# Kernel optimization log

Hardware: AMD Instinct MI355X
Metric: run time of the kernel (lower is better)

## Reference

```python
import jax, jax.numpy as jnp
import numpy as np

NEG_INF = -1e9
B, D, T_MEL, T_TEXT = 16, 192, 2048, 512


def setup_inputs() -> dict:
    key = jax.random.key(0)
    k1, k2, k3, k4, k5 = jax.random.split(key, 5)
    z_p = jax.random.normal(k1, (B, D, T_MEL), dtype=jnp.float32)
    m_p = jax.random.normal(k2, (B, D, T_TEXT), dtype=jnp.float32)
    logs_p = 0.1 * jax.random.normal(k3, (B, D, T_TEXT), dtype=jnp.float32)
    phoneme_lengths = jax.random.randint(k4, (B,), T_TEXT // 2, T_TEXT + 1, dtype=jnp.int32)
    mel_lengths = jax.random.randint(k5, (B,), T_MEL // 2, T_MEL + 1, dtype=jnp.int32)
    return {"z_p": z_p, "m_p": m_p, "logs_p": logs_p,
            "phoneme_lengths": phoneme_lengths, "mel_lengths": mel_lengths}


def neg_cent_matrix(z_p, m_p, logs_p):
    # z_p: [B,D,Ty] (mel frames), m_p/logs_p: [B,D,Tx] (phonemes)
    s = jnp.exp(-2.0 * logs_p)                                             # 1/sigma^2, [B,D,Tx]
    nc1 = jnp.sum(-0.5 * jnp.log(2.0 * jnp.pi) - logs_p, axis=1, keepdims=True)  # [B,1,Tx]
    nc2 = jnp.einsum('bdy,bdx->byx', -0.5 * z_p * z_p, s)                  # [B,Ty,Tx]
    nc3 = jnp.einsum('bdy,bdx->byx', z_p, m_p * s)                         # [B,Ty,Tx]
    nc4 = jnp.sum(-0.5 * m_p * m_p * s, axis=1, keepdims=True)             # [B,1,Tx]
    return nc1 + nc2 + nc3 + nc4                                           # [B,Ty,Tx]


def maximum_path(neg_cent, t_xs, t_ys):
    """Monotonic alignment search (VITS maximum_path), vmapped over batch.

    neg_cent: [B, T_y, T_x] log-likelihood scores; t_xs/t_ys: valid lengths.
    Returns hard alignment path [B, T_y, T_x] in {0,1}.
    """
    _, T_y, T_x = neg_cent.shape
    x_idx = jnp.arange(T_x)

    def single(value, t_x, t_y):
        # forward DP: cum[y,x] = value[y,x] + max(cum[y-1,x], cum[y-1,x-1])
        init = jnp.where(x_idx == 0, value[0], NEG_INF)

        def fwd_step(prev, v_row):
            shifted = jnp.concatenate([jnp.full((1,), NEG_INF, prev.dtype), prev[:-1]])
            cur = v_row + jnp.maximum(prev, shifted)
            return cur, cur

        _, rest = jax.lax.scan(fwd_step, init, value[1:])
        cum = jnp.concatenate([init[None, :], rest], axis=0)               # [T_y,T_x]

        # backtrack from (t_y-1, t_x-1); rows with y >= t_y are inactive (zeros)
        def bwd_step(index, y):
            active = y < t_y
            row = ((x_idx == index) & active).astype(value.dtype)
            prev_row = cum[jnp.maximum(y - 1, 0)]
            move = (index == y) | (prev_row[index] < prev_row[jnp.maximum(index - 1, 0)])
            move = move & (index > 0) & active & (y > 0)
            nxt = jnp.where(active, index - move.astype(index.dtype), index)
            return nxt, row

        _, rows = jax.lax.scan(bwd_step, t_x - 1, jnp.arange(T_y)[::-1])
        return rows[::-1]

    return jax.vmap(single)(neg_cent, t_xs, t_ys)


def reference(z_p, m_p, logs_p, phoneme_lengths, mel_lengths):
    neg_cent = neg_cent_matrix(z_p, m_p, logs_p)                           # [B,Ty,Tx]
    attn = maximum_path(neg_cent, phoneme_lengths, mel_lengths)            # [B,Ty,Tx]
    T_x = m_p.shape[-1]
    ph_mask = (jnp.arange(T_x)[None, :] < phoneme_lengths[:, None]).astype(z_p.dtype)[:, None, :]  # [B,1,Tx]
    w = jnp.sum(attn, axis=1)[:, None, :]                                  # durations, [B,1,Tx]
    logw_ = jnp.log(w + 1e-6) * ph_mask                                    # [B,1,Tx]
    return neg_cent, attn, logw_
```

## Files before the change

### kernel.cpp

```cpp
#include <hip/hip_runtime.h>
#include <cstdint>
#include <cstddef>

#define B_   16
#define D_   192
#define TY   2048
#define TX   512
#define NEG_INF_F (-1e9f)

#define CHUNK 16
#define RING  4
#define WAVES 8

#define WAITVM(N)  __builtin_amdgcn_s_waitcnt(((N) & 15) | (7 << 4) | (15 << 8) | (((N) >> 4) << 14))
#define WAITLGKM0  __builtin_amdgcn_s_waitcnt(15 | (7 << 4) | (0 << 8) | (3 << 14))

__device__ __forceinline__ void gload_lds16(const float* g, float* l) {
    __builtin_amdgcn_global_load_lds(
        (const __attribute__((address_space(1))) void*)g,
        (__attribute__((address_space(3))) void*)l, 16, 0, 0);
}

__device__ __forceinline__ float dpp_shr1_neginf(float x) {
    int xi  = __builtin_bit_cast(int, x);
    int old = __builtin_bit_cast(int, NEG_INF_F);
    int r = __builtin_amdgcn_update_dpp(old, xi, 0x138, 0xF, 0xF, false);
    return __builtin_bit_cast(float, r);
}

__global__ __launch_bounds__(256)
void nc14_kernel(const float* __restrict__ m_p,
                 const float* __restrict__ logs_p,
                 float* __restrict__ nc14) {
    int gid = blockIdx.x * 256 + threadIdx.x;
    int b = gid >> 9;
    int x = gid & 511;
    const float c = -0.9189385332046727f;
    const float* lp = logs_p + (size_t)b * D_ * TX + x;
    const float* mp = m_p    + (size_t)b * D_ * TX + x;
    float acc1 = 0.f, acc2 = 0.f;
    for (int d = 0; d < D_; ++d) {
        float l = lp[(size_t)d * TX];
        float m = mp[(size_t)d * TX];
        float s = __expf(-2.f * l);
        acc1 += c - l;
        acc2 += m * m * s;
    }
    nc14[gid] = acc1 - 0.5f * acc2;
}

#define BM 128
#define BN 128
#define BK 16
#define PADF 4

__global__ __launch_bounds__(256)
void gemm_kernel(const float* __restrict__ z_p,
                 const float* __restrict__ m_p,
                 const float* __restrict__ logs_p,
                 const float* __restrict__ nc14,
                 float* __restrict__ out) {
    __shared__ float a_z [BK][BM + PADF];
    __shared__ float a_z2[BK][BM + PADF];
    __shared__ float sb_s [BK][BN + PADF];
    __shared__ float sb_ms[BK][BN + PADF];

    const int b  = blockIdx.z;
    const int m0 = blockIdx.y * BM;
    const int n0 = blockIdx.x * BN;
    const int tid = threadIdx.x;
    const int tx2 = tid & 15;
    const int ty2 = tid >> 4;

    const int skk = tid >> 4;
    const int sy  = (tid & 15) * 8;

    const float* zb = z_p    + (size_t)b * D_ * TY;
    const float* mb = m_p    + (size_t)b * D_ * TX;
    const float* lb = logs_p + (size_t)b * D_ * TX;

    float acc[8][8];
    #pragma unroll
    for (int i = 0; i < 8; ++i)
        #pragma unroll
        for (int j = 0; j < 8; ++j) acc[i][j] = 0.f;

    float4 va0, va1, vl0, vl1, vm0, vm1;
    auto ld = [&](int k0) {
        const float* zr = zb + (size_t)(k0 + skk) * TY + m0 + sy;
        const float* lr = lb + (size_t)(k0 + skk) * TX + n0 + sy;
        const float* mr = mb + (size_t)(k0 + skk) * TX + n0 + sy;
        va0 = *(const float4*)zr;       va1 = *(const float4*)(zr + 4);
        vl0 = *(const float4*)lr;       vl1 = *(const float4*)(lr + 4);
        vm0 = *(const float4*)mr;       vm1 = *(const float4*)(mr + 4);
    };
    auto st = [&]() {
        *(float4*)&a_z[skk][sy]     = va0;
        *(float4*)&a_z[skk][sy + 4] = va1;
        float4 w0, w1;
        w0.x = -0.5f * va0.x * va0.x; w0.y = -0.5f * va0.y * va0.y;
        w0.z = -0.5f * va0.z * va0.z; w0.w = -0.5f * va0.w * va0.w;
        w1.x = -0.5f * va1.x * va1.x; w1.y = -0.5f * va1.y * va1.y;
        w1.z = -0.5f * va1.z * va1.z; w1.w = -0.5f * va1.w * va1.w;
        *(float4*)&a_z2[skk][sy]     = w0;
        *(float4*)&a_z2[skk][sy + 4] = w1;
        float4 s0, s1;
        s0.x = __expf(-2.f * vl0.x); s0.y = __expf(-2.f * vl0.y);
        s0.z = __expf(-2.f * vl0.z); s0.w = __expf(-2.f * vl0.w);
        s1.x = __expf(-2.f * vl1.x); s1.y = __expf(-2.f * vl1.y);
        s1.z = __expf(-2.f * vl1.z); s1.w = __expf(-2.f * vl1.w);
        *(float4*)&sb_s[skk][sy]     = s0;
        *(float4*)&sb_s[skk][sy + 4] = s1;
        float4 q0, q1;
        q0.x = vm0.x * s0.x; q0.y = vm0.y * s0.y;
        q0.z = vm0.z * s0.z; q0.w = vm0.w * s0.w;
        q1.x = vm1.x * s1.x; q1.y = vm1.y * s1.y;
        q1.z = vm1.z * s1.z; q1.w = vm1.w * s1.w;
        *(float4*)&sb_ms[skk][sy]     = q0;
        *(float4*)&sb_ms[skk][sy + 4] = q1;
    };

    ld(0);
    for (int k0 = 0; k0 < D_; k0 += BK) {
        st();
        __syncthreads();
        if (k0 + BK < D_) ld(k0 + BK);
        #pragma unroll 4
        for (int kk = 0; kk < BK; ++kk) {
            float az[8], a2[8], bs[8], bm[8];
            *(float4*)&az[0] = *(const float4*)&a_z [kk][ty2 * 8];
            *(float4*)&az[4] = *(const float4*)&a_z [kk][ty2 * 8 + 4];
            *(float4*)&a2[0] = *(const float4*)&a_z2[kk][ty2 * 8];
            *(float4*)&a2[4] = *(const float4*)&a_z2[kk][ty2 * 8 + 4];
            *(float4*)&bs[0] = *(const float4*)&sb_s [kk][tx2 * 8];
            *(float4*)&bs[4] = *(const float4*)&sb_s [kk][tx2 * 8 + 4];
            *(float4*)&bm[0] = *(const float4*)&sb_ms[kk][tx2 * 8];
            *(float4*)&bm[4] = *(const float4*)&sb_ms[kk][tx2 * 8 + 4];
            #pragma unroll
            for (int i = 0; i < 8; ++i)
                #pragma unroll
                for (int j = 0; j < 8; ++j)
                    acc[i][j] += a2[i] * bs[j] + az[i] * bm[j];
        }
        __syncthreads();
    }
    const float4 c4a = *(const float4*)(nc14 + b * TX + n0 + tx2 * 8);
    const float4 c4b = *(const float4*)(nc14 + b * TX + n0 + tx2 * 8 + 4);
    float* ob = out + (size_t)b * TY * TX + (size_t)m0 * TX + n0 + tx2 * 8;
    #pragma unroll
    for (int i = 0; i < 8; ++i) {
        float4 r0, r1;
        r0.x = acc[i][0] + c4a.x; r0.y = acc[i][1] + c4a.y;
        r0.z = acc[i][2] + c4a.z; r0.w = acc[i][3] + c4a.w;
        r1.x = acc[i][4] + c4b.x; r1.y = acc[i][5] + c4b.y;
        r1.z = acc[i][6] + c4b.z; r1.w = acc[i][7] + c4b.w;
        float* op = ob + (size_t)(ty2 * 8 + i) * TX;
        *(float4*)op       = r0;
        *(float4*)(op + 4) = r1;
    }
}

__global__ __launch_bounds__(512, 1)
void dp_kernel(float* __restrict__ out,
               const int* __restrict__ t_xs,
               const int* __restrict__ t_ys,
               int* __restrict__ cumE) {
    const size_t PLANE = (size_t)TY * TX;
    const size_t OFF1  = (size_t)B_ * PLANE;
    const size_t OFF2  = 2 * OFF1;

    __shared__ float rows_lds[WAVES][RING][CHUNK * 64];
    __shared__ float bnd[RING][WAVES + 1][CHUNK];
    __shared__ int   w_lds[TX];

    const int b    = blockIdx.x;
    const int tid  = threadIdx.x;
    const int w    = tid >> 6;
    const int lane = tid & 63;
    const int t_x  = t_xs[b];
    const int t_y  = t_ys[b];
    const int tym1 = t_y - 1;
    const int NC   = (t_y + CHUNK - 1) / CHUNK;

    const float* nc   = out + (size_t)b * PLANE;
    float*       attn = out + OFF1 + (size_t)b * PLANE;
    float*       logw = out + OFF2 + (size_t)b * TX;
    unsigned char* bitsb = (unsigned char*)attn;

    w_lds[tid] = 0;
    {
        float* bf = &bnd[0][0][0];
        if (tid < 512) bf[tid] = NEG_INF_F;
        if (tid < 64)  bf[512 + tid] = NEG_INF_F;
    }

    auto issue_chunk = [&](int c) {
        const int slot = c % RING;
        #pragma unroll
        for (int k = 0; k < CHUNK / 4; ++k) {
            int y = c * CHUNK + 4 * k + (lane >> 4);
            if (y > tym1) y = tym1;
            const float* gp = nc + (size_t)y * TX + 64 * w + 4 * (lane & 15);
            gload_lds16(gp, &rows_lds[w][slot][k * 256]);
        }
    };

    float cl = NEG_INF_F;
    const bool lane0  = (lane == 0);
    const bool lane63 = (lane == 63);

    issue_chunk(0);
    issue_chunk(1);
    issue_chunk(2);

    float vvA[CHUNK], vvB[CHUNK];
    float carryA = NEG_INF_F, carryB = NEG_INF_F;
    #pragma unroll
    for (int r = 0; r < CHUNK; ++r) { vvA[r] = 0.f; vvB[r] = 0.f; }

    if (w == 0) {
        WAITVM(8);
        __asm__ volatile("" ::: "memory");
        const float* vn = &rows_lds[0][0][0];
        #pragma unroll
        for (int r = 0; r < CHUNK; ++r) vvA[r] = vn[r * 64 + lane];
        #pragma unroll
        for (int r = 0; r < CHUNK; ++r) __asm__ volatile("" : "+v"(vvA[r]));
    }

    const int ITERS = NC + WAVES - 1;

    auto body = [&](float (&vvc)[CHUNK], float& carryc,
                    float (&vvn)[CHUNK], float& carryn, int i) {
        WAITLGKM0;
        __asm__ volatile("" ::: "memory");
        __builtin_amdgcn_s_barrier();
        __asm__ volatile("" ::: "memory");
        const int c = i - w;
        if (c >= 0 && c < NC) {
            if (c + 3 < NC) issue_chunk(c + 3);
            const int pc = c % RING;
            float4 bq0 = *(const float4*)&bnd[pc][w][0];
            float4 bq1 = *(const float4*)&bnd[pc][w][4];
            float4 bq2 = *(const float4*)&bnd[pc][w][8];
            float4 bq3 = *(const float4*)&bnd[pc][w][12];

            const int ybase = c * CHUNK;
            float pub[CHUNK];
            unsigned mlo = 0, mhi = 0;
            {
                float sh = dpp_shr1_neginf(cl);
                sh = lane0 ? carryc : sh;
                unsigned long long mk = __ballot(cl < sh);
                float cn = vvc[0] + fmaxf(cl, sh);
                if (ybase == 0)
                    cn = (w == 0 && lane0) ? vvc[0] : NEG_INF_F;
                cl = cn;
                pub[0] = cl;
                bool sel = (lane == 0);
                mlo = sel ? (unsigned)mk : mlo;
                mhi = sel ? (unsigned)(mk >> 32) : mhi;
            }
            float bv1[CHUNK - 1] = {bq0.x, bq0.y, bq0.z, bq0.w,
                                    bq1.x, bq1.y, bq1.z, bq1.w,
                                    bq2.x, bq2.y, bq2.z, bq2.w,
                                    bq3.x, bq3.y, bq3.z};
            #pragma unroll
            for (int r = 1; r < CHUNK; ++r) {
                float sh = dpp_shr1_neginf(cl);
                sh = lane0 ? bv1[r - 1] : sh;
                unsigned long long mk = __ballot(cl < sh);
                float cn = vvc[r] + fmaxf(cl, sh);
                cl = cn;
                pub[r] = cl;
                bool sel = (lane == r);
                mlo = sel ? (unsigned)mk : mlo;
                mhi = sel ? (unsigned)(mk >> 32) : mhi;
            }
            if (lane63) {
                *(float4*)&bnd[pc][w + 1][0]  = make_float4(pub[0],  pub[1],  pub[2],  pub[3]);
                *(float4*)&bnd[pc][w + 1][4]  = make_float4(pub[4],  pub[5],  pub[6],  pub[7]);
                *(float4*)&bnd[pc][w + 1][8]  = make_float4(pub[8],  pub[9],  pub[10], pub[11]);
                *(float4*)&bnd[pc][w + 1][12] = make_float4(pub[12], pub[13], pub[14], pub[15]);
            }
            {
                const int ys = ybase + lane;
                if (lane < CHUNK && ys < t_y)
                    *(uint2*)(bitsb + (size_t)ys * 64 + 8 * w) = make_uint2(mlo, mhi);
            }
        }
        const int cp = (i - w) + 1;
        if (cp >= 0 && cp < NC) {
            const int cc = cp - 1;
            if (cp == 0)            { WAITVM(8);  }
            else if (cp == 1)       { WAITVM(9);  }
            else if (cp == 2)       { WAITVM(10); }
            else if (cc + 4 <= NC)  { WAITVM(11); }
            else if (cc + 3 == NC)  { WAITVM(7);  }
            else                    { WAITVM(3);  }
            __asm__ volatile("" ::: "memory");
            const float* vn = &rows_lds[w][cp % RING][0];
            #pragma unroll
            for (int r = 0; r < CHUNK; ++r) vvn[r] = vn[r * 64 + lane];
            carryn = bnd[(cp + RING - 1) % RING][w][CHUNK - 1];
            #pragma unroll
            for (int r = 0; r < CHUNK; ++r) __asm__ volatile("" : "+v"(vvn[r]));
            __asm__ volatile("" : "+v"(carryn));
        }
    };

    {
        int i = 0;
        while (i < ITERS) {
            body(vvA, carryA, vvB, carryB, i); ++i;
            if (i >= ITERS) break;
            body(vvB, carryB, vvA, carryA, i); ++i;
        }
    }

    __builtin_amdgcn_s_waitcnt(0);
    __asm__ volatile("" ::: "memory");
    __builtin_amdgcn_s_barrier();
    __asm__ volatile("" ::: "memory");
    if (w != 0) return;

    int idx  = t_x - 1;
    int yhi  = tym1;
    int ytop = tym1;
    int wh   = idx >> 5;

    unsigned vlo = 0, vhi = 0;
    {
        int cnt0 = (ytop >= 31) ? 32 : (ytop + 1);
        int wlo = (wh > 0) ? wh - 1 : 0;
        if (lane < cnt0) {
            const unsigned* rp = (const unsigned*)(bitsb + (size_t)(ytop - lane) * 64);
            vlo = rp[wlo];
            vhi = rp[wh];
        }
    }
    while (ytop >= 0) {
        const int cnt = (ytop >= 31) ? 32 : (ytop + 1);
        unsigned p0 = 0, p1 = 0, p2 = 0;
        const int ynext = ytop - cnt;
        if (ynext >= 0 && lane < 32) {
            int rr = ynext - lane; if (rr < 0) rr = 0;
            const unsigned* rp = (const unsigned*)(bitsb + (size_t)rr * 64);
            const int w2i = wh;
            const int w1i = (wh > 0) ? wh - 1 : 0;
            const int w0i = (wh > 1) ? wh - 2 : 0;
            p0 = rp[w0i]; p1 = rp[w1i]; p2 = rp[w2i];
        }
        const int base  = ((wh > 0) ? wh - 1 : 0) * 32;
        const int idx0  = idx;
        const int yhi0  = yhi;
        unsigned  mask  = 0;
        auto step = [&](int i2) {
            int yy = ytop - i2;
            unsigned lo = (unsigned)__builtin_amdgcn_readlane((int)vlo, i2);
            unsigned hi = (unsigned)__builtin_amdgcn_readlane((int)vhi, i2);
            unsigned long long V = ((unsigned long long)hi << 32) | lo;
            int pos   = idx - base;
            int bit   = (int)((V >> pos) & 1ull);
            int force = (idx == yy) ? 1 : 0;
            int move  = (force | bit) & ((idx > 0) ? 1 : 0) & ((yy > 0) ? 1 : 0);
            mask |= ((unsigned)move) << i2;
            yhi  = move ? (yy - 1) : yhi;
            idx -= move;
        };
        if (cnt == 32) {
            #pragma unroll
            for (int i2 = 0; i2 < 32; ++i2) step(i2);
        } else {
            for (int i2 = 0; i2 < cnt; ++i2) step(i2);
        }
        {
            const int k = lane;
            if (k < 32 && ((mask >> k) & 1u)) {
                unsigned pri = mask & ((1u << k) - 1u);
                int m  = __popc(pri);
                int ph = idx0 - m;
                int dur;
                if (pri) { int kp = 31 - __builtin_clz(pri); dur = k - kp; }
                else     { dur = yhi0 - ytop + k + 1; }
                w_lds[ph] = dur;
            }
        }
        ytop -= cnt;
        if (ytop >= 0) {
            const int whn = idx >> 5;
            vlo = (whn == wh) ? p1 : p0;
            vhi = (whn == wh) ? p2 : p1;
            wh = whn;
        }
    }
    if (lane0) w_lds[idx] = yhi + 1;

    __asm__ volatile("" ::: "memory");
    int v2[8];
    int run = 0;
    #pragma unroll
    for (int j = 0; j < 8; ++j) {
        int wv = w_lds[lane * 8 + j];
        run += wv;
        v2[j] = run;
    }
    int off = run;
    #pragma unroll
    for (int d = 1; d < 64; d <<= 1) {
        int t = __shfl_up(off, d, 64);
        if (lane >= d) off += t;
    }
    int excl = off - run;
    #pragma unroll
    for (int j = 0; j < 8; ++j) {
        int x = lane * 8 + j;
        cumE[b * TX + x] = v2[j] + excl;
        int wv = w_lds[x];
        logw[x] = (x < t_x) ? logf((float)wv + 1e-6f) : 0.f;
    }
}

__global__ __launch_bounds__(256)
void attn_fill_kernel(const int* __restrict__ cumE,
                      float* __restrict__ out) {
    const size_t PLANE = (size_t)TY * TX;
    const size_t OFF1  = (size_t)B_ * PLANE;
    __shared__ int cs[TX + 1];
    const int b  = blockIdx.y;
    const int y0 = blockIdx.x * 4;
    const int t  = threadIdx.x;
    if (t == 0) cs[0] = 0;
    cs[1 + t]       = cumE[b * TX + t];
    cs[1 + 256 + t] = cumE[b * TX + 256 + t];
    __syncthreads();
    const int y  = y0 + (t >> 6);
    const int x0 = (t & 63) * 8;
    float r[8];
    #pragma unroll
    for (int j = 0; j < 8; ++j)
        r[j] = (cs[x0 + j] <= y && y < cs[x0 + j + 1]) ? 1.f : 0.f;
    float* p = out + OFF1 + (size_t)b * PLANE + (size_t)y * TX + x0;
    *(float4*)p       = *(float4*)&r[0];
    *(float4*)(p + 4) = *(float4*)&r[4];
}

extern "C" void kernel_launch(void* const* d_in, const int* in_sizes, int n_in,
                              void* d_out, int out_size, void* d_ws, size_t ws_size,
                              hipStream_t stream) {
    const float* z_p    = (const float*)d_in[0];
    const float* m_p    = (const float*)d_in[1];
    const float* logs_p = (const float*)d_in[2];
    const int* ph_len   = (const int*)d_in[3];
    const int* mel_len  = (const int*)d_in[4];
    float* out  = (float*)d_out;
    float* nc14 = (float*)d_ws;
    int*   cumE = (int*)d_ws;

    nc14_kernel<<<(B_ * TX) / 256, 256, 0, stream>>>(m_p, logs_p, nc14);
    gemm_kernel<<<dim3(TX / BN, TY / BM, B_), 256, 0, stream>>>(z_p, m_p, logs_p, nc14, out);
    dp_kernel<<<B_, WAVES * 64, 0, stream>>>(out, ph_len, mel_len, cumE);
    attn_fill_kernel<<<dim3(TY / 4, B_), 256, 0, stream>>>(cumE, out);
}
```

Baseline: 620.9 us.

## Prefetch DP score rows straight into registers with triple buffering

The DP kernel no longer stages neg_cent rows through an LDS ring with global_load_lds. Each wave now loads its 16-row chunk directly into one of three rotating register arrays, two chunks ahead, and the vmcnt waits are retuned to match. This removes the LDS write and read round trip, and the shared buffer, from the serial per-chunk critical path. In exchange it costs extra VGPRs, uses a shallower prefetch distance, and drops the row clamping, so it now reads real but unused rows past t_y.

```diff
diff --git a/kernel.cpp b/kernel.cpp
--- a/kernel.cpp
+++ b/kernel.cpp
@@ -14,12 +14,6 @@
 
 #define WAITVM(N)  __builtin_amdgcn_s_waitcnt(((N) & 15) | (7 << 4) | (15 << 8) | (((N) >> 4) << 14))
 #define WAITLGKM0  __builtin_amdgcn_s_waitcnt(15 | (7 << 4) | (0 << 8) | (3 << 14))
-
-__device__ __forceinline__ void gload_lds16(const float* g, float* l) {
-    __builtin_amdgcn_global_load_lds(
-        (const __attribute__((address_space(1))) void*)g,
-        (__attribute__((address_space(3))) void*)l, 16, 0, 0);
-}
 
 __device__ __forceinline__ float dpp_shr1_neginf(float x) {
     int xi  = __builtin_bit_cast(int, x);
@@ -169,7 +163,6 @@
     const size_t OFF1  = (size_t)B_ * PLANE;
     const size_t OFF2  = 2 * OFF1;
 
-    __shared__ float rows_lds[WAVES][RING][CHUNK * 64];
     __shared__ float bnd[RING][WAVES + 1][CHUNK];
     __shared__ int   w_lds[TX];
 
@@ -194,51 +187,45 @@
         if (tid < 64)  bf[512 + tid] = NEG_INF_F;
     }
 
-    auto issue_chunk = [&](int c) {
-        const int slot = c % RING;
+    auto issue_rows = [&](int c, float (&dst)[CHUNK]) {
+        const float* gp = nc + (size_t)(c * CHUNK) * TX + 64 * w + lane;
         #pragma unroll
-        for (int k = 0; k < CHUNK / 4; ++k) {
-            int y = c * CHUNK + 4 * k + (lane >> 4);
-            if (y > tym1) y = tym1;
-            const float* gp = nc + (size_t)y * TX + 64 * w + 4 * (lane & 15);
-            gload_lds16(gp, &rows_lds[w][slot][k * 256]);
-        }
+        for (int r = 0; r < CHUNK; ++r) dst[r] = gp[(size_t)r * TX];
+        __asm__ volatile("" ::: "memory");
     };
 
     float cl = NEG_INF_F;
     const bool lane0  = (lane == 0);
     const bool lane63 = (lane == 63);
 
-    issue_chunk(0);
-    issue_chunk(1);
-    issue_chunk(2);
-
-    float vvA[CHUNK], vvB[CHUNK];
-    float carryA = NEG_INF_F, carryB = NEG_INF_F;
-    #pragma unroll
-    for (int r = 0; r < CHUNK; ++r) { vvA[r] = 0.f; vvB[r] = 0.f; }
-
+    float vb0[CHUNK], vb1[CHUNK], vb2[CHUNK];
+    float cy0 = NEG_INF_F, cy1 = NEG_INF_F, cy2 = NEG_INF_F;
+    #pragma unroll
+    for (int r = 0; r < CHUNK; ++r) { vb0[r] = 0.f; vb1[r] = 0.f; vb2[r] = 0.f; }
+
+    switch (w % 3) {
+        case 0: issue_rows(0, vb1); issue_rows(1, vb2); break;
+        case 1: issue_rows(0, vb2); issue_rows(1, vb0); break;
+        default: issue_rows(0, vb0); issue_rows(1, vb1); break;
+    }
     if (w == 0) {
-        WAITVM(8);
+        WAITVM(16);
         __asm__ volatile("" ::: "memory");
-        const float* vn = &rows_lds[0][0][0];
         #pragma unroll
-        for (int r = 0; r < CHUNK; ++r) vvA[r] = vn[r * 64 + lane];
-        #pragma unroll
-        for (int r = 0; r < CHUNK; ++r) __asm__ volatile("" : "+v"(vvA[r]));
+        for (int r = 0; r < CHUNK; ++r) __asm__ volatile("" : "+v"(vb1[r]));
     }
 
     const int ITERS = NC + WAVES - 1;
 
-    auto body = [&](float (&vvc)[CHUNK], float& carryc,
-                    float (&vvn)[CHUNK], float& carryn, int i) {
+    auto body = [&](float (&iss)[CHUNK], float (&cons)[CHUNK], float (&flt)[CHUNK],
+                    float& cyc, float& cyf, int i) {
         WAITLGKM0;
         __asm__ volatile("" ::: "memory");
         __builtin_amdgcn_s_barrier();
         __asm__ volatile("" ::: "memory");
         const int c = i - w;
+        if (i >= w && c + 2 < NC) issue_rows(c + 2, iss);
         if (c >= 0 && c < NC) {
-            if (c + 3 < NC) issue_chunk(c + 3);
             const int pc = c % RING;
             float4 bq0 = *(const float4*)&bnd[pc][w][0];
             float4 bq1 = *(const float4*)&bnd[pc][w][4];
@@ -250,11 +237,11 @@
             unsigned mlo = 0, mhi = 0;
             {
                 float sh = dpp_shr1_neginf(cl);
-                sh = lane0 ? carryc : sh;
+                sh = lane0 ? cyc : sh;
                 unsigned long long mk = __ballot(cl < sh);
-                float cn = vvc[0] + fmaxf(cl, sh);
+                float cn = cons[0] + fmaxf(cl, sh);
                 if (ybase == 0)
-                    cn = (w == 0 && lane0) ? vvc[0] : NEG_INF_F;
+                    cn = (w == 0 && lane0) ? cons[0] : NEG_INF_F;
                 cl = cn;
                 pub[0] = cl;
                 bool sel = (lane == 0);
@@ -270,7 +257,7 @@
                 float sh = dpp_shr1_neginf(cl);
                 sh = lane0 ? bv1[r - 1] : sh;
                 unsigned long long mk = __ballot(cl < sh);
-                float cn = vvc[r] + fmaxf(cl, sh);
+                float cn = cons[r] + fmaxf(cl, sh);
                 cl = cn;
                 pub[r] = cl;
                 bool sel = (lane == r);
@@ -289,33 +276,24 @@
                     *(uint2*)(bitsb + (size_t)ys * 64 + 8 * w) = make_uint2(mlo, mhi);
             }
         }
-        const int cp = (i - w) + 1;
+        const int cp = c + 1;
         if (cp >= 0 && cp < NC) {
-            const int cc = cp - 1;
-            if (cp == 0)            { WAITVM(8);  }
-            else if (cp == 1)       { WAITVM(9);  }
-            else if (cp == 2)       { WAITVM(10); }
-            else if (cc + 4 <= NC)  { WAITVM(11); }
-            else if (cc + 3 == NC)  { WAITVM(7);  }
-            else                    { WAITVM(3);  }
+            if (cp == 0)           { WAITVM(16); }
+            else if (cp == 1)      { WAITVM(17); }
+            else if (c + 2 < NC)   { WAITVM(18); }
+            else                   { WAITVM(2);  }
             __asm__ volatile("" ::: "memory");
-            const float* vn = &rows_lds[w][cp % RING][0];
             #pragma unroll
-            for (int r = 0; r < CHUNK; ++r) vvn[r] = vn[r * 64 + lane];
-            carryn = bnd[(cp + RING - 1) % RING][w][CHUNK - 1];
-            #pragma unroll
-            for (int r = 0; r < CHUNK; ++r) __asm__ volatile("" : "+v"(vvn[r]));
-            __asm__ volatile("" : "+v"(carryn));
+            for (int r = 0; r < CHUNK; ++r) __asm__ volatile("" : "+v"(flt[r]));
+            cyf = bnd[(cp + RING - 1) % RING][w][CHUNK - 1];
+            __asm__ volatile("" : "+v"(cyf));
         }
     };
 
-    {
-        int i = 0;
-        while (i < ITERS) {
-            body(vvA, carryA, vvB, carryB, i); ++i;
-            if (i >= ITERS) break;
-            body(vvB, carryB, vvA, carryA, i); ++i;
-        }
+    for (int i = 0; i < ITERS; i += 3) {
+        body(vb0, vb1, vb2, cy1, cy2, i);
+        body(vb1, vb2, vb0, cy2, cy0, i + 1);
+        body(vb2, vb0, vb1, cy0, cy1, i + 2);
     }
 
     __builtin_amdgcn_s_waitcnt(0);
```

Result: slower. 652.2 us (+5.0%).

## Replace block-wide barriers in wavefront DP with per-wave LDS flag handoff

Applied to the files above, without the earlier changes.

The forward DP pipeline used to advance all 8 waves in lockstep, with an s_barrier on every diagonal step. It now has each wave spin on volatile LDS sequence counters: one that its left neighbour bumps when it publishes boundary values, and one the consumer bumps to release ring slots back to the producer. This drops the global barrier and the software double-buffered register prefetch, so waves can run ahead independently. The cost is spin-wait polling of LDS and simpler, non-prefetched LDS loads of each chunk's rows, plus a risk of memory-ordering issues between waves.

```diff
diff --git a/kernel.cpp b/kernel.cpp
--- a/kernel.cpp
+++ b/kernel.cpp
@@ -171,7 +171,12 @@
 
     __shared__ float rows_lds[WAVES][RING][CHUNK * 64];
     __shared__ float bnd[RING][WAVES + 1][CHUNK];
+    __shared__ int   seqf[WAVES + 1];
+    __shared__ int   cseqf[WAVES + 1];
     __shared__ int   w_lds[TX];
+
+    volatile int* seqv  = seqf;
+    volatile int* cseqv = cseqf;
 
     const int b    = blockIdx.x;
     const int tid  = threadIdx.x;
@@ -187,15 +192,8 @@
     float*       logw = out + OFF2 + (size_t)b * TX;
     unsigned char* bitsb = (unsigned char*)attn;
 
-    w_lds[tid] = 0;
-    {
-        float* bf = &bnd[0][0][0];
-        if (tid < 512) bf[tid] = NEG_INF_F;
-        if (tid < 64)  bf[512 + tid] = NEG_INF_F;
-    }
-
     auto issue_chunk = [&](int c) {
-        const int slot = c % RING;
+        const int slot = c & (RING - 1);
         #pragma unroll
         for (int k = 0; k < CHUNK / 4; ++k) {
             int y = c * CHUNK + 4 * k + (lane >> 4);
@@ -205,116 +203,99 @@
         }
     };
 
-    float cl = NEG_INF_F;
-    const bool lane0  = (lane == 0);
-    const bool lane63 = (lane == 63);
-
     issue_chunk(0);
     issue_chunk(1);
     issue_chunk(2);
 
-    float vvA[CHUNK], vvB[CHUNK];
-    float carryA = NEG_INF_F, carryB = NEG_INF_F;
-    #pragma unroll
-    for (int r = 0; r < CHUNK; ++r) { vvA[r] = 0.f; vvB[r] = 0.f; }
-
-    if (w == 0) {
-        WAITVM(8);
+    w_lds[tid] = 0;
+    {
+        float* bf = &bnd[0][0][0];
+        if (tid < 512) bf[tid] = NEG_INF_F;
+        if (tid < 64)  bf[512 + tid] = NEG_INF_F;
+    }
+    if (tid <= WAVES) { seqf[tid] = 0; cseqf[tid] = 0; }
+    WAITLGKM0;
+    __asm__ volatile("" ::: "memory");
+    __builtin_amdgcn_s_barrier();
+    __asm__ volatile("" ::: "memory");
+
+    float cl    = NEG_INF_F;
+    float carry = NEG_INF_F;
+    const bool lane0  = (lane == 0);
+    const bool lane63 = (lane == 63);
+
+    for (int c = 0; c < NC; ++c) {
+        const int sl = c & (RING - 1);
+        if (c + 3 < NC) issue_chunk(c + 3);
+
+        if (c == 0)           { WAITVM(12); }
+        else if (c == 1)      { WAITVM(13); }
+        else if (c == 2)      { WAITVM(14); }
+        else if (c + 3 < NC)  { WAITVM(15); }
+        else if (c + 3 == NC) { WAITVM(11); }
+        else if (c + 2 == NC) { WAITVM(7);  }
+        else                  { WAITVM(3);  }
         __asm__ volatile("" ::: "memory");
-        const float* vn = &rows_lds[0][0][0];
+
+        const float* vrow = &rows_lds[w][sl][0];
+        float vv[CHUNK];
         #pragma unroll
-        for (int r = 0; r < CHUNK; ++r) vvA[r] = vn[r * 64 + lane];
-        #pragma unroll
-        for (int r = 0; r < CHUNK; ++r) __asm__ volatile("" : "+v"(vvA[r]));
-    }
-
-    const int ITERS = NC + WAVES - 1;
-
-    auto body = [&](float (&vvc)[CHUNK], float& carryc,
-                    float (&vvn)[CHUNK], float& carryn, int i) {
+        for (int r = 0; r < CHUNK; ++r) vv[r] = vrow[r * 64 + lane];
+
+        if (w > 0) { while (seqv[w] < c + 1) { } }
+        __asm__ volatile("" ::: "memory");
+        float4 bq0 = *(const float4*)&bnd[sl][w][0];
+        float4 bq1 = *(const float4*)&bnd[sl][w][4];
+        float4 bq2 = *(const float4*)&bnd[sl][w][8];
+        float4 bq3 = *(const float4*)&bnd[sl][w][12];
         WAITLGKM0;
         __asm__ volatile("" ::: "memory");
-        __builtin_amdgcn_s_barrier();
-        __asm__ volatile("" ::: "memory");
-        const int c = i - w;
-        if (c >= 0 && c < NC) {
-            if (c + 3 < NC) issue_chunk(c + 3);
-            const int pc = c % RING;
-            float4 bq0 = *(const float4*)&bnd[pc][w][0];
-            float4 bq1 = *(const float4*)&bnd[pc][w][4];
-            float4 bq2 = *(const float4*)&bnd[pc][w][8];
-            float4 bq3 = *(const float4*)&bnd[pc][w][12];
-
-            const int ybase = c * CHUNK;
-            float pub[CHUNK];
-            unsigned mlo = 0, mhi = 0;
-            {
-                float sh = dpp_shr1_neginf(cl);
-                sh = lane0 ? carryc : sh;
-                unsigned long long mk = __ballot(cl < sh);
-                float cn = vvc[0] + fmaxf(cl, sh);
-                if (ybase == 0)
-                    cn = (w == 0 && lane0) ? vvc[0] : NEG_INF_F;
-                cl = cn;
-                pub[0] = cl;
-                bool sel = (lane == 0);
-                mlo = sel ? (unsigned)mk : mlo;
-                mhi = sel ? (unsigned)(mk >> 32) : mhi;
+        if (w > 0 && lane63) cseqv[w] = c + 1;
+
+        const int ybase = c * CHUNK;
+        float bv[CHUNK] = {carry,
+                           bq0.x, bq0.y, bq0.z, bq0.w,
+                           bq1.x, bq1.y, bq1.z, bq1.w,
+                           bq2.x, bq2.y, bq2.z, bq2.w,
+                           bq3.x, bq3.y, bq3.z};
+        carry = bq3.w;
+        float pub[CHUNK];
+        unsigned mlo = 0, mhi = 0;
+        #pragma unroll
+        for (int r = 0; r < CHUNK; ++r) {
+            float sh = dpp_shr1_neginf(cl);
+            sh = lane0 ? bv[r] : sh;
+            unsigned long long mk = __ballot(cl < sh);
+            float cn = vv[r] + fmaxf(cl, sh);
+            if (r == 0) {
+                float iv = (w == 0 && lane0) ? vv[0] : NEG_INF_F;
+                cn = (ybase == 0) ? iv : cn;
             }
-            float bv1[CHUNK - 1] = {bq0.x, bq0.y, bq0.z, bq0.w,
-                                    bq1.x, bq1.y, bq1.z, bq1.w,
-                                    bq2.x, bq2.y, bq2.z, bq2.w,
-                                    bq3.x, bq3.y, bq3.z};
-            #pragma unroll
-            for (int r = 1; r < CHUNK; ++r) {
-                float sh = dpp_shr1_neginf(cl);
-                sh = lane0 ? bv1[r - 1] : sh;
-                unsigned long long mk = __ballot(cl < sh);
-                float cn = vvc[r] + fmaxf(cl, sh);
-                cl = cn;
-                pub[r] = cl;
-                bool sel = (lane == r);
-                mlo = sel ? (unsigned)mk : mlo;
-                mhi = sel ? (unsigned)(mk >> 32) : mhi;
+            cl = cn;
+            pub[r] = cl;
+            bool sel = (lane == r);
+            mlo = sel ? (unsigned)mk : mlo;
+            mhi = sel ? (unsigned)(mk >> 32) : mhi;
+        }
+
+        if (w < WAVES - 1) {
+            if (c >= RING) { while (cseqv[w + 1] < c - (RING - 1)) { } }
+            __asm__ volatile("" ::: "memory");
+            if (lane63) {
+                *(float4*)&bnd[sl][w + 1][0]  = make_float4(pub[0],  pub[1],  pub[2],  pub[3]);
+                *(float4*)&bnd[sl][w + 1][4]  = make_float4(pub[4],  pub[5],  pub[6],  pub[7]);
+                *(float4*)&bnd[sl][w + 1][8]  = make_float4(pub[8],  pub[9],  pub[10], pub[11]);
+                *(float4*)&bnd[sl][w + 1][12] = make_float4(pub[12], pub[13], pub[14], pub[15]);
             }
-            if (lane63) {
-                *(float4*)&bnd[pc][w + 1][0]  = make_float4(pub[0],  pub[1],  pub[2],  pub[3]);
-                *(float4*)&bnd[pc][w + 1][4]  = make_float4(pub[4],  pub[5],  pub[6],  pub[7]);
-                *(float4*)&bnd[pc][w + 1][8]  = make_float4(pub[8],  pub[9],  pub[10], pub[11]);
-                *(float4*)&bnd[pc][w + 1][12] = make_float4(pub[12], pub[13], pub[14], pub[15]);
-            }
-            {
-                const int ys = ybase + lane;
-                if (lane < CHUNK && ys < t_y)
-                    *(uint2*)(bitsb + (size_t)ys * 64 + 8 * w) = make_uint2(mlo, mhi);
-            }
-        }
-        const int cp = (i - w) + 1;
-        if (cp >= 0 && cp < NC) {
-            const int cc = cp - 1;
-            if (cp == 0)            { WAITVM(8);  }
-            else if (cp == 1)       { WAITVM(9);  }
-            else if (cp == 2)       { WAITVM(10); }
-            else if (cc + 4 <= NC)  { WAITVM(11); }
-            else if (cc + 3 == NC)  { WAITVM(7);  }
-            else                    { WAITVM(3);  }
+            WAITLGKM0;
             __asm__ volatile("" ::: "memory");
-            const float* vn = &rows_lds[w][cp % RING][0];
-            #pragma unroll
-            for (int r = 0; r < CHUNK; ++r) vvn[r] = vn[r * 64 + lane];
-            carryn = bnd[(cp + RING - 1) % RING][w][CHUNK - 1];
-            #pragma unroll
-            for (int r = 0; r < CHUNK; ++r) __asm__ volatile("" : "+v"(vvn[r]));
-            __asm__ volatile("" : "+v"(carryn));
-        }
-    };
-
-    {
-        int i = 0;
-        while (i < ITERS) {
-            body(vvA, carryA, vvB, carryB, i); ++i;
-            if (i >= ITERS) break;
-            body(vvB, carryB, vvA, carryA, i); ++i;
+            if (lane63) seqv[w + 1] = c + 1;
+        }
+
+        {
+            const int ys = ybase + lane;
+            if (lane < CHUNK && ys < t_y)
+                *(uint2*)(bitsb + (size_t)ys * 64 + 8 * w) = make_uint2(mlo, mhi);
         }
     }
 
```

Measured after the change: 635.6 us. +2.4%, slower.
